# Kernel tuning notes

Hardware: AMD Instinct MI355X
Metric: run time of the kernel (lower is better)

## Reference

```python
import jax, jax.numpy as jnp
import numpy as np
import math

ATTN_C = 32
HEADS = 8
IN_C = 256
PAIR_C = 128
B, M, N = 1, 128, 256


def _layernorm(x, w, b, eps=1e-5):
    mu = jnp.mean(x, axis=-1, keepdims=True)
    xc = x - mu
    var = jnp.mean(xc * xc, axis=-1, keepdims=True)
    return xc * jax.lax.rsqrt(var + eps) * w + b


def setup_inputs() -> dict:
    key = jax.random.key(0)
    ks = jax.random.split(key, 10)
    s1 = 1.0 / math.sqrt(IN_C)
    s2 = 1.0 / math.sqrt(PAIR_C)
    s3 = 1.0 / math.sqrt(ATTN_C * HEADS)
    return {
        "x1d": jax.random.normal(ks[0], (B, M, N, IN_C), jnp.float32),
        "x2d": jax.random.normal(ks[1], (B, N, N, PAIR_C), jnp.float32),
        "norm_w": jnp.ones((IN_C,), jnp.float32),
        "norm_b": jnp.zeros((IN_C,), jnp.float32),
        "qkv_w": jax.random.normal(ks[2], (3 * ATTN_C * HEADS, IN_C), jnp.float32) * s1,
        "x2d_w": jax.random.normal(ks[3], (HEADS, PAIR_C), jnp.float32) * s2,
        "gate_w": jax.random.normal(ks[4], (ATTN_C * HEADS, IN_C), jnp.float32) * s1,
        "gate_b": jnp.zeros((ATTN_C * HEADS,), jnp.float32),
        "final_w": jax.random.normal(ks[5], (IN_C, ATTN_C * HEADS), jnp.float32) * s3,
        "final_b": jnp.zeros((IN_C,), jnp.float32),
    }


def reference(x1d, x2d, norm_w, norm_b, qkv_w, x2d_w, gate_w, gate_b, final_w, final_b):
    c, h = ATTN_C, HEADS
    x = _layernorm(x1d, norm_w, norm_b)                      # [B,M,N,IN_C]
    qkv = (x @ qkv_w.T).reshape(*x.shape[:-1], c, 3 * h)     # [B,M,N,c,3h]
    q, k, v = qkv[..., :h], qkv[..., h:2 * h], qkv[..., 2 * h:]
    aff = jnp.einsum('bmich,bmjch->bmijh', q, k)             # [B,M,N,N,H]
    gate = jax.nn.sigmoid(x @ gate_w.T + gate_b).reshape(*x.shape[:-1], c, h)
    factor = 1.0 / math.sqrt(c)
    bias = (x2d @ x2d_w.T) * factor                          # [B,N,N,H]
    weights = jax.nn.softmax(aff + bias[:, None], axis=-2)   # softmax over j
    out = jnp.einsum('bmrch,bmirh->bmich', v, weights) * gate
    out = out.reshape(*x.shape[:-1], c * h) @ final_w.T + final_b
    return out
```

## Files before the change

kernel.cpp:

```cpp
#include <hip/hip_runtime.h>
#include <math.h>

typedef short bf16x8 __attribute__((ext_vector_type(8)));
typedef float f32x4  __attribute__((ext_vector_type(4)));

#define NPOS 32768
#define LOG2E 1.4426950408889634f

#define OFF_AHI   100663296u
#define OFF_ATTN  134217728u
#define OFF_BIAST 150994944u
#define OFF_WHI   153354240u
#define OFF_W2P   154402816u
#define OFF_GBP   154533888u

__device__ __forceinline__ short f2bf(float x) {
    unsigned int u = __float_as_uint(x);
    unsigned int r = (u + 0x7FFFu + ((u >> 16) & 1u)) >> 16;
    return (short)r;
}
__device__ __forceinline__ float bf2f(short s) {
    return __uint_as_float(((unsigned int)(unsigned short)s) << 16);
}
__device__ __forceinline__ void async_copy16(const void* g, void* l) {
    __builtin_amdgcn_global_load_lds(
        (const __attribute__((address_space(1))) unsigned int*)g,
        (__attribute__((address_space(3))) unsigned int*)l, 16, 0, 0);
}

#define PREP_LN   8192
#define PREP_CW   9473
__global__ __launch_bounds__(256) void k_prep(
    const float* __restrict__ x, const float* __restrict__ nw, const float* __restrict__ nb,
    const float* __restrict__ qkvw, const float* __restrict__ gatew,
    const float* __restrict__ gateb, const float* __restrict__ finalw,
    const float* __restrict__ x2d, const float* __restrict__ x2dw,
    short* __restrict__ Ahi, short* __restrict__ Whi, short* __restrict__ W2p,
    float* __restrict__ gbp, float* __restrict__ biasT) {
    __shared__ float xs[64][132];
    __shared__ float ws[8][132];
    const int bid = blockIdx.x;
    const int t = threadIdx.x;

    if (bid < PREP_LN) {
        int wid = (bid * 256 + t) >> 6;
        int lane = t & 63;
        const float4 v = ((const float4*)(x + (size_t)wid * 256))[lane];
        float s  = v.x + v.y + v.z + v.w;
        float ss = v.x*v.x + v.y*v.y + v.z*v.z + v.w*v.w;
        #pragma unroll
        for (int o = 32; o; o >>= 1) {
            s  += __shfl_xor(s,  o, 64);
            ss += __shfl_xor(ss, o, 64);
        }
        float mu  = s * (1.0f / 256);
        float var = ss * (1.0f / 256) - mu * mu;
        float rs  = rsqrtf(var + 1e-5f);
        const float4 wv = ((const float4*)nw)[lane];
        const float4 bv = ((const float4*)nb)[lane];
        float y[4] = {(v.x - mu) * rs * wv.x + bv.x, (v.y - mu) * rs * wv.y + bv.y,
                      (v.z - mu) * rs * wv.z + bv.z, (v.w - mu) * rs * wv.w + bv.w};
        short h4[4];
        #pragma unroll
        for (int i = 0; i < 4; ++i) h4[i] = f2bf(y[i]);
        *(short4*)(Ahi + (size_t)wid * 256 + lane * 4) = *(short4*)h4;
    } else if (bid < PREP_CW) {
        int r = bid - PREP_LN;
        if (r < 1024) {
            int which = r >> 8, h = (r >> 5) & 7, c = r & 31;
            const float* src = (which < 3) ? qkvw + (size_t)(c * 24 + which * 8 + h) * 256
                                           : gatew + (size_t)(c * 8 + h) * 256;
            Whi[(size_t)r * 256 + t] = f2bf(src[t]);
        } else if (r < 1280) {
            int o = r - 1024;
            int h = t >> 5, c = t & 31;
            W2p[(size_t)o * 256 + t] = f2bf(finalw[(size_t)o * 256 + c * 8 + h]);
        } else {
            int h = t >> 5, c = t & 31;
            gbp[t] = gateb[c * 8 + h];
        }
    } else {
        const int wid0 = (bid - PREP_CW) * 64;
        #pragma unroll
        for (int r = 0; r < 8; ++r) {
            int g = r * 256 + t;
            int row = g >> 5, c4 = g & 31;
            float4 v = *(const float4*)(x2d + (size_t)(wid0 + row) * 128 + c4 * 4);
            *(float4*)&xs[row][c4 * 4] = v;
        }
        {
            int h = t >> 5, c4 = t & 31;
            *(float4*)&ws[h][c4 * 4] = *(const float4*)(x2dw + h * 128 + c4 * 4);
        }
        __syncthreads();
        const float f = 0.17677669529663687f * LOG2E;
        const int i = wid0 >> 8;
        #pragma unroll
        for (int kk = 0; kk < 2; ++kk) {
            int o = t + kk * 256;
            int row = o >> 3, h = o & 7;
            float acc = 0.f;
            #pragma unroll
            for (int c4 = 0; c4 < 32; ++c4) {
                float4 xv = *(const float4*)&xs[row][c4 * 4];
                float4 wv = *(const float4*)&ws[h][c4 * 4];
                acc += xv.x * wv.x + xv.y * wv.y + xv.z * wv.z + xv.w * wv.w;
            }
            int j = (wid0 & 255) + row;
            biasT[(((h * 256 + j)) << 8) + i] = acc * f;
        }
    }
}

__global__ __launch_bounds__(512, 4) void k_fused(
    const short* __restrict__ Ahi, const short* __restrict__ Whi,
    const float* __restrict__ gbp, const float* __restrict__ biasT,
    short* __restrict__ attnB) {
    __shared__ __align__(16) short smem[38144];
    short* As  = smem;
    short* Ws  = smem + 16384;
    short* Khi = smem;
    short* VT  = smem + 8192;
    short* Qs  = smem + 16640;
    short* Gs  = smem + 24832;
    short* Pl  = smem + 33024;

    const int mh = blockIdx.x;
    const int h = mh >> 7, m = mh & 127;
    const int t = threadIdx.x;
    const int wave = t >> 6, lane = t & 63, ln15 = lane & 15, quad = lane >> 4;
    const int i0 = wave * 32;

    f32x4 acc[2][8];
    #pragma unroll
    for (int a = 0; a < 2; ++a)
        #pragma unroll
        for (int b = 0; b < 8; ++b) acc[a][b] = (f32x4){0.f, 0.f, 0.f, 0.f};

    for (int k0 = 0; k0 < 256; k0 += 64) {
        #pragma unroll
        for (int r = 0; r < 4; ++r) {
            int g = r * 512 + t;
            int row = g >> 3, cs = g & 7;
            int colg = cs ^ (row & 7);
            async_copy16(Ahi + (size_t)(m * 256 + row) * 256 + k0 + colg * 8, &As[g * 8]);
        }
        #pragma unroll
        for (int r = 0; r < 2; ++r) {
            int g = r * 512 + t;
            int row = g >> 3, cs = g & 7;
            int colg = cs ^ (row & 7);
            int nrow = (row >> 5) * 256 + h * 32 + (row & 31);
            async_copy16(Whi + (size_t)nrow * 256 + k0 + colg * 8, &Ws[g * 8]);
        }
        __syncthreads();
        #pragma unroll
        for (int kc = 0; kc < 2; ++kc) {
            bf16x8 af[2], bfr[8];
            #pragma unroll
            for (int it = 0; it < 2; ++it) {
                int rowa = i0 + it * 16 + ln15;
                int c8a = (kc * 4 + quad) ^ (rowa & 7);
                af[it] = *(const bf16x8*)&As[rowa * 64 + c8a * 8];
            }
            #pragma unroll
            for (int nt = 0; nt < 8; ++nt) {
                int rowb = nt * 16 + ln15;
                int c8b = (kc * 4 + quad) ^ (rowb & 7);
                bfr[nt] = *(const bf16x8*)&Ws[rowb * 64 + c8b * 8];
            }
            #pragma unroll
            for (int it = 0; it < 2; ++it)
                #pragma unroll
                for (int nt = 0; nt < 8; ++nt)
                    acc[it][nt] = __builtin_amdgcn_mfma_f32_16x16x32_bf16(
                        bfr[nt], af[it], acc[it][nt], 0, 0, 0);
        }
        __syncthreads();
    }

    #pragma unroll
    for (int it = 0; it < 2; ++it) {
        int j = i0 + it * 16 + ln15;
        int sw = j & 3;
        #pragma unroll
        for (int nt = 0; nt < 8; ++nt) {
            int which = nt >> 1;
            int cloc0 = (nt & 1) * 16 + quad * 4;
            float v0 = acc[it][nt][0], v1 = acc[it][nt][1];
            float v2 = acc[it][nt][2], v3 = acc[it][nt][3];
            if (which == 3) {
                const float4 gb = *(const float4*)&gbp[h * 32 + cloc0];
                v0 = 1.0f / (1.0f + __expf(-(v0 + gb.x)));
                v1 = 1.0f / (1.0f + __expf(-(v1 + gb.y)));
                v2 = 1.0f / (1.0f + __expf(-(v2 + gb.z)));
                v3 = 1.0f / (1.0f + __expf(-(v3 + gb.w)));
            }
            short s0 = f2bf(v0), s1 = f2bf(v1), s2 = f2bf(v2), s3 = f2bf(v3);
            if (which == 2) {
                VT[(cloc0 + 0) * 264 + j] = s0;
                VT[(cloc0 + 1) * 264 + j] = s1;
                VT[(cloc0 + 2) * 264 + j] = s2;
                VT[(cloc0 + 3) * 264 + j] = s3;
            } else {
                unsigned w0 = (unsigned)(unsigned short)s0 | ((unsigned)(unsigned short)s1 << 16);
                unsigned w1 = (unsigned)(unsigned short)s2 | ((unsigned)(unsigned short)s3 << 16);
                int cg = cloc0 >> 3, off = cloc0 & 7;
                short* dst = (which == 0) ? &Qs[j * 32 + (cg ^ sw) * 8 + off]
                           : (which == 1) ? &Khi[j * 32 + (cg ^ sw) * 8 + off]
                                          : &Gs[j * 32 + cloc0];
                *(uint2*)dst = make_uint2(w0, w1);
            }
        }
    }
    __syncthreads();

    bf16x8 qhi[2];
    #pragma unroll
    for (int it = 0; it < 2; ++it) {
        int i = i0 + it * 16 + ln15;
        qhi[it] = *(const bf16x8*)&Qs[i * 32 + ((quad ^ (i & 3))) * 8];
    }
    float lacc[2] = {0.f, 0.f};
    f32x4 Oacc[2][2];
    #pragma unroll
    for (int a = 0; a < 2; ++a) {
        Oacc[a][0] = (f32x4){0.f, 0.f, 0.f, 0.f};
        Oacc[a][1] = (f32x4){0.f, 0.f, 0.f, 0.f};
    }
    const float* bp = biasT + (size_t)h * 65536;

    for (int j0 = 0; j0 < 256; j0 += 32) {
        bf16x8 kfh[2], vf[2];
        #pragma unroll
        for (int jt = 0; jt < 2; ++jt) {
            int j = j0 + jt * 16 + ln15;
            int cs = quad ^ (j & 3);
            kfh[jt] = *(const bf16x8*)&Khi[j * 32 + cs * 8];
        }
        #pragma unroll
        for (int ct = 0; ct < 2; ++ct) {
            int c = ct * 16 + ln15;
            vf[ct] = *(const bf16x8*)&VT[c * 264 + j0 + quad * 8];
        }
        #pragma unroll
        for (int it = 0; it < 2; ++it) {
            int i = i0 + it * 16 + ln15;
            float b0[4], b1[4];
            #pragma unroll
            for (int r = 0; r < 4; ++r) {
                b0[r] = bp[(j0 + quad * 4 + r) * 256 + i];
                b1[r] = bp[(j0 + 16 + quad * 4 + r) * 256 + i];
            }
            f32x4 s0 = (f32x4){0.f, 0.f, 0.f, 0.f};
            f32x4 s1 = (f32x4){0.f, 0.f, 0.f, 0.f};
            __builtin_amdgcn_s_setprio(1);
            s0 = __builtin_amdgcn_mfma_f32_16x16x32_bf16(kfh[0], qhi[it], s0, 0, 0, 0);
            s1 = __builtin_amdgcn_mfma_f32_16x16x32_bf16(kfh[1], qhi[it], s1, 0, 0, 0);
            __builtin_amdgcn_s_setprio(0);
            float p[8], ps = 0.f;
            #pragma unroll
            for (int r = 0; r < 4; ++r) {
                p[r] = __builtin_amdgcn_exp2f(fmaf(s0[r], LOG2E, b0[r]));
                ps += p[r];
            }
            #pragma unroll
            for (int r = 0; r < 4; ++r) {
                p[4 + r] = __builtin_amdgcn_exp2f(fmaf(s1[r], LOG2E, b1[r]));
                ps += p[4 + r];
            }
            lacc[it] += ps;
            unsigned long long pw0 =
                  (unsigned long long)(unsigned short)f2bf(p[0])
                | ((unsigned long long)(unsigned short)f2bf(p[1]) << 16)
                | ((unsigned long long)(unsigned short)f2bf(p[2]) << 32)
                | ((unsigned long long)(unsigned short)f2bf(p[3]) << 48);
            unsigned long long pw1 =
                  (unsigned long long)(unsigned short)f2bf(p[4])
                | ((unsigned long long)(unsigned short)f2bf(p[5]) << 16)
                | ((unsigned long long)(unsigned short)f2bf(p[6]) << 32)
                | ((unsigned long long)(unsigned short)f2bf(p[7]) << 48);
            short* plp = &Pl[(wave * 16 + ln15) * 40];
            *(unsigned long long*)&plp[quad * 4]      = pw0;
            *(unsigned long long*)&plp[16 + quad * 4] = pw1;
            bf16x8 pf = *(const bf16x8*)&plp[quad * 8];
            __builtin_amdgcn_s_setprio(1);
            Oacc[it][0] = __builtin_amdgcn_mfma_f32_16x16x32_bf16(pf, vf[0], Oacc[it][0], 0, 0, 0);
            Oacc[it][1] = __builtin_amdgcn_mfma_f32_16x16x32_bf16(pf, vf[1], Oacc[it][1], 0, 0, 0);
            __builtin_amdgcn_s_setprio(0);
        }
    }
    #pragma unroll
    for (int it = 0; it < 2; ++it) {
        float l = lacc[it];
        l += __shfl_xor(l, 16, 64);
        l += __shfl_xor(l, 32, 64);
        float inv = 1.0f / l;
        float invr[4];
        #pragma unroll
        for (int r = 0; r < 4; ++r) invr[r] = __shfl(inv, quad * 4 + r, 16);
        #pragma unroll
        for (int ct = 0; ct < 2; ++ct) {
            int c = ct * 16 + ln15;
            #pragma unroll
            for (int r = 0; r < 4; ++r) {
                int i = i0 + it * 16 + quad * 4 + r;
                float g = bf2f(Gs[i * 32 + c]);
                float val = Oacc[it][ct][r] * invr[r] * g;
                attnB[(size_t)(m * 256 + i) * 256 + h * 32 + c] = f2bf(val);
            }
        }
    }
}

__global__ __launch_bounds__(256) void k_gemm2m(
    const short* __restrict__ A, const short* __restrict__ W2p,
    const float* __restrict__ fb, float* __restrict__ out) {
    __shared__ short As[128 * 64];
    __shared__ short Bs[128 * 64];
    const int t = threadIdx.x;
    const int wave = t >> 6, lane = t & 63, ln15 = lane & 15, quad = lane >> 4;
    const int posBase = blockIdx.x * 128;
    const int nb = blockIdx.y;
    const int i0w = (wave & 1) * 64, n0w = (wave >> 1) * 64;

    f32x4 acc[4][4];
    #pragma unroll
    for (int a = 0; a < 4; ++a)
        #pragma unroll
        for (int b = 0; b < 4; ++b) acc[a][b] = (f32x4){0.f, 0.f, 0.f, 0.f};

    for (int k0 = 0; k0 < 256; k0 += 64) {
        #pragma unroll
        for (int r = 0; r < 4; ++r) {
            int g = r * 256 + t;
            int row = g >> 3, cs = g & 7;
            int colg = cs ^ (row & 7);
            const short* ga = A + (size_t)(posBase + row) * 256 + k0 + colg * 8;
            async_copy16(ga, &As[(r * 256 + wave * 64) * 8]);
            const short* gb = W2p + (size_t)(nb * 128 + row) * 256 + k0 + colg * 8;
            async_copy16(gb, &Bs[(r * 256 + wave * 64) * 8]);
        }
        __syncthreads();
        #pragma unroll
        for (int kc = 0; kc < 2; ++kc) {
            bf16x8 af[4], bfr[4];
            #pragma unroll
            for (int it = 0; it < 4; ++it) {
                int rowa = i0w + it * 16 + ln15;
                int c8a = (kc * 4 + quad) ^ (rowa & 7);
                af[it] = *(const bf16x8*)&As[rowa * 64 + c8a * 8];
                int rowb = n0w + it * 16 + ln15;
                int c8b = (kc * 4 + quad) ^ (rowb & 7);
                bfr[it] = *(const bf16x8*)&Bs[rowb * 64 + c8b * 8];
            }
            #pragma unroll
            for (int it = 0; it < 4; ++it)
                #pragma unroll
                for (int nt = 0; nt < 4; ++nt)
                    acc[it][nt] = __builtin_amdgcn_mfma_f32_16x16x32_bf16(
                        bfr[nt], af[it], acc[it][nt], 0, 0, 0);
        }
        __syncthreads();
    }
    #pragma unroll
    for (int it = 0; it < 4; ++it) {
        size_t pos = posBase + i0w + it * 16 + ln15;
        #pragma unroll
        for (int nt = 0; nt < 4; ++nt) {
            int ncol0 = nb * 128 + n0w + nt * 16 + quad * 4;
            const float4 fbv = *(const float4*)&fb[ncol0];
            float4 o;
            o.x = acc[it][nt][0] + fbv.x;
            o.y = acc[it][nt][1] + fbv.y;
            o.z = acc[it][nt][2] + fbv.z;
            o.w = acc[it][nt][3] + fbv.w;
            *(float4*)&out[pos * 256 + ncol0] = o;
        }
    }
}

extern "C" void kernel_launch(void* const* d_in, const int* in_sizes, int n_in,
                              void* d_out, int out_size, void* d_ws, size_t ws_size,
                              hipStream_t stream) {
    const float* x1d     = (const float*)d_in[0];
    const float* x2d     = (const float*)d_in[1];
    const float* norm_w  = (const float*)d_in[2];
    const float* norm_b  = (const float*)d_in[3];
    const float* qkv_w   = (const float*)d_in[4];
    const float* x2d_w   = (const float*)d_in[5];
    const float* gate_w  = (const float*)d_in[6];
    const float* gate_b  = (const float*)d_in[7];
    const float* final_w = (const float*)d_in[8];
    const float* final_b = (const float*)d_in[9];
    float* out = (float*)d_out;
    char* w = (char*)d_ws;

    short* Ahi   = (short*)(w + OFF_AHI);
    short* attnB = (short*)(w + OFF_ATTN);
    float* biasT = (float*)(w + OFF_BIAST);
    short* Whi   = (short*)(w + OFF_WHI);
    short* W2p   = (short*)(w + OFF_W2P);
    float* gbp   = (float*)(w + OFF_GBP);

    k_prep<<<10497, 256, 0, stream>>>(x1d, norm_w, norm_b, qkv_w, gate_w, gate_b,
                                      final_w, x2d, x2d_w, Ahi, Whi, W2p, gbp, biasT);
    k_fused<<<1024, 512, 0, stream>>>(Ahi, Whi, gbp, biasT, attnB);
    k_gemm2m<<<dim3(256, 2), 256, 0, stream>>>(attnB, W2p, final_b, out);
}
```

Measured before the change: 193.1 us.

## Double-buffer A tiles in fused QKV GEMM to overlap loads with MFMA

Splits the A-operand shared buffer into two halves so the next K-slice of activations is fetched asynchronously while the current slice is multiplied. W tiles stay single-buffered and are reloaded after the trailing barrier. Explicit vmcnt waits and raw s_barrier replace __syncthreads. Shared memory grows from about 76KB to 80KB per block, which may cut occupancy, and the hand-counted vmcnt values must match the number of outstanding copies.

```diff
diff --git a/kernel.cpp b/kernel.cpp
--- a/kernel.cpp
+++ b/kernel.cpp
@@ -116,9 +116,10 @@
     const short* __restrict__ Ahi, const short* __restrict__ Whi,
     const float* __restrict__ gbp, const float* __restrict__ biasT,
     short* __restrict__ attnB) {
-    __shared__ __align__(16) short smem[38144];
-    short* As  = smem;
-    short* Ws  = smem + 16384;
+    __shared__ __align__(16) short smem[40960];
+    short* As0 = smem;
+    short* As1 = smem + 16384;
+    short* Ws  = smem + 32768;
     short* Khi = smem;
     short* VT  = smem + 8192;
     short* Qs  = smem + 16640;
@@ -137,14 +138,16 @@
         #pragma unroll
         for (int b = 0; b < 8; ++b) acc[a][b] = (f32x4){0.f, 0.f, 0.f, 0.f};
 
-    for (int k0 = 0; k0 < 256; k0 += 64) {
+    auto stageA = [&](short* buf, int k0) {
         #pragma unroll
         for (int r = 0; r < 4; ++r) {
             int g = r * 512 + t;
             int row = g >> 3, cs = g & 7;
             int colg = cs ^ (row & 7);
-            async_copy16(Ahi + (size_t)(m * 256 + row) * 256 + k0 + colg * 8, &As[g * 8]);
-        }
+            async_copy16(Ahi + (size_t)(m * 256 + row) * 256 + k0 + colg * 8, &buf[g * 8]);
+        }
+    };
+    auto stageW = [&](int k0) {
         #pragma unroll
         for (int r = 0; r < 2; ++r) {
             int g = r * 512 + t;
@@ -153,7 +156,22 @@
             int nrow = (row >> 5) * 256 + h * 32 + (row & 31);
             async_copy16(Whi + (size_t)nrow * 256 + k0 + colg * 8, &Ws[g * 8]);
         }
-        __syncthreads();
+    };
+
+    stageA(As0, 0);
+    stageW(0);
+    #pragma unroll
+    for (int ks = 0; ks < 4; ++ks) {
+        short* cur = (ks & 1) ? As1 : As0;
+        if (ks < 3) {
+            stageA((ks & 1) ? As0 : As1, (ks + 1) * 64);
+            asm volatile("s_waitcnt vmcnt(4)" ::: "memory");
+        } else {
+            asm volatile("s_waitcnt vmcnt(0)" ::: "memory");
+        }
+        __builtin_amdgcn_sched_barrier(0);
+        __builtin_amdgcn_s_barrier();
+        __builtin_amdgcn_sched_barrier(0);
         #pragma unroll
         for (int kc = 0; kc < 2; ++kc) {
             bf16x8 af[2], bfr[8];
@@ -161,7 +179,7 @@
             for (int it = 0; it < 2; ++it) {
                 int rowa = i0 + it * 16 + ln15;
                 int c8a = (kc * 4 + quad) ^ (rowa & 7);
-                af[it] = *(const bf16x8*)&As[rowa * 64 + c8a * 8];
+                af[it] = *(const bf16x8*)&cur[rowa * 64 + c8a * 8];
             }
             #pragma unroll
             for (int nt = 0; nt < 8; ++nt) {
@@ -176,7 +194,10 @@
                     acc[it][nt] = __builtin_amdgcn_mfma_f32_16x16x32_bf16(
                         bfr[nt], af[it], acc[it][nt], 0, 0, 0);
         }
-        __syncthreads();
+        __builtin_amdgcn_sched_barrier(0);
+        __builtin_amdgcn_s_barrier();
+        __builtin_amdgcn_sched_barrier(0);
+        if (ks < 3) stageW((ks + 1) * 64);
     }
 
     #pragma unroll
```

After: 196.6 us. Within noise of the previous version (+1.8%).
